# Kernel optimization log

Hardware: AMD Instinct MI355X
Metric: run time of the kernel (lower is better)

Reference implementation:

```python
import jax, jax.numpy as jnp
import numpy as np
from jax import lax

GN_GROUPS = 32
EPS = 1e-5


def conv_gn_silu(x, W, b, scale, bias, stride, padding):
    # Conv2d (OIHW weights, NCHW data) -> GroupNorm(32) -> SiLU
    y = lax.conv_general_dilated(
        x, W, (stride, stride), [(padding, padding), (padding, padding)],
        dimension_numbers=("NCHW", "OIHW", "NCHW")) + b[None, :, None, None]
    B, C, H, Wd = y.shape
    yr = y.reshape(B, GN_GROUPS, C // GN_GROUPS, H, Wd)
    mu = yr.mean(axis=(2, 3, 4), keepdims=True)
    var = yr.var(axis=(2, 3, 4), keepdims=True)
    yn = ((yr - mu) * lax.rsqrt(var + EPS)).reshape(B, C, H, Wd)
    yn = yn * scale[None, :, None, None] + bias[None, :, None, None]
    return yn * jax.nn.sigmoid(yn)  # SiLU


def setup_inputs() -> dict:
    key = jax.random.key(0)
    ks = jax.random.split(key, 8)
    C = 256
    B, H, W = 8, 64, 64
    f = lambda k, shp, s: jax.random.normal(k, shp, dtype=jnp.float32) * s
    return {
        "x": f(ks[0], (B, C, H, W), 1.0),
        "y": f(ks[1], (B, C, H, W), 1.0),
        "Wq": f(ks[2], (C, C, 3, 3), 0.02),
        "bq": jnp.zeros((C,), jnp.float32),
        "gq_scale": jnp.ones((C,), jnp.float32),
        "gq_bias": jnp.zeros((C,), jnp.float32),
        "Wk": f(ks[3], (C, C, 2, 2), 0.02),
        "bk": jnp.zeros((C,), jnp.float32),
        "gk_scale": jnp.ones((C,), jnp.float32),
        "gk_bias": jnp.zeros((C,), jnp.float32),
        "Wv": f(ks[4], (C, C, 2, 2), 0.02),
        "bv": jnp.zeros((C,), jnp.float32),
        "gv_scale": jnp.ones((C,), jnp.float32),
        "gv_bias": jnp.zeros((C,), jnp.float32),
        "gamma": f(ks[5], (1,), 1.0),
    }


def reference(x, y, Wq, bq, gq_scale, gq_bias, Wk, bk, gk_scale, gk_bias,
              Wv, bv, gv_scale, gv_bias, gamma):
    B, C, H, W = x.shape
    sr = 2
    Cq = C  # in_dim // factor, factor=1
    q = conv_gn_silu(x, Wq, bq, gq_scale, gq_bias, stride=1, padding=1)   # [B,Cq,H,W]
    k = conv_gn_silu(y, Wk, bk, gk_scale, gk_bias, stride=sr, padding=0)  # [B,Cq,H/sr,W/sr]
    v = conv_gn_silu(y, Wv, bv, gv_scale, gv_bias, stride=sr, padding=0)  # [B,C,H/sr,W/sr]
    N = H * W
    M = (H // sr) * (W // sr)
    q = q.reshape(B, Cq, N)   # proj_query (pre-permute)
    k = k.reshape(B, Cq, M)   # proj_key
    v = v.reshape(B, C, M)    # proj_value
    scale = 1.0 / np.sqrt(Cq).astype(np.float32)
    energy = jnp.einsum("bcn,bcm->bnm", q, k) * scale       # [B,N,M]
    attn = jax.nn.softmax(energy, axis=-1)                   # softmax over keys
    out = jnp.einsum("bcm,bnm->bcn", v, attn).reshape(B, C, H, W)
    return gamma * out
```

## Files before the change

kernel.cpp:

```cpp
#include <hip/hip_runtime.h>
#include <hip/hip_bf16.h>
#include <math.h>

#define B_ 8
#define C_ 256
#define H_ 64
#define W_ 64
#define N_ 4096
#define M_ 1024
#define HW_ 4096

typedef __attribute__((ext_vector_type(8))) short short8;
typedef __attribute__((ext_vector_type(4))) float f32x4;

__device__ __forceinline__ unsigned short f2bf(float x) {
    unsigned u = __float_as_uint(x);
    u += 0x7fffu + ((u >> 16) & 1u);
    return (unsigned short)(u >> 16);
}
__device__ __forceinline__ float bf2f(unsigned short h) {
    return __uint_as_float(((unsigned)h) << 16);
}

__device__ __forceinline__ void gl_lds16(const unsigned short* g, unsigned short* l) {
    __builtin_amdgcn_global_load_lds(
        (const __attribute__((address_space(1))) unsigned int*)g,
        (__attribute__((address_space(3))) unsigned int*)l, 16, 0, 0);
}

__global__ __launch_bounds__(256) void split_w_tap(
    const float* __restrict__ Wq, unsigned short* __restrict__ wtH,
    unsigned short* __restrict__ wtL)
{
    int co = blockIdx.x, ci = threadIdx.x;
    const float* wp = Wq + ((size_t)co * 256 + ci) * 9;
    #pragma unroll
    for (int tap = 0; tap < 9; ++tap) {
        float v = wp[tap];
        unsigned short h = f2bf(v), l = f2bf(v - bf2f(h));
        size_t o = ((size_t)tap << 16) + ((size_t)co << 8) + ci;
        wtH[o] = h; wtL[o] = l;
    }
}

__global__ __launch_bounds__(256) void split_w2(
    const float* __restrict__ Wsrc, unsigned short* __restrict__ wH,
    unsigned short* __restrict__ wL)
{
    int co = blockIdx.x, ci = threadIdx.x;
    const float* wp = Wsrc + ((size_t)co * 256 + ci) * 4;
    #pragma unroll
    for (int tap = 0; tap < 4; ++tap) {
        float v = wp[tap];
        unsigned short h = f2bf(v), l = f2bf(v - bf2f(h));
        size_t o = ((size_t)tap << 16) + ((size_t)co << 8) + ci;
        wH[o] = h; wL[o] = l;
    }
}

__global__ __launch_bounds__(256) void split_x_pad(
    const float* __restrict__ x, unsigned short* __restrict__ xpH,
    unsigned short* __restrict__ xpL)
{
    __shared__ float tile[64][65];
    int blk = blockIdx.x;
    int b = blk >> 6, h = blk & 63;
    int t = threadIdx.x;
    const float* xb = x + ((size_t)b << 20) + (size_t)h * 64;
    size_t obase = (((size_t)b * 4356) + (size_t)(h + 1) * 66 + 1) * 256;
    unsigned short* oH = xpH + obase;
    unsigned short* oL = xpL + obase;
    for (int cc = 0; cc < 256; cc += 64) {
        int wi = t & 63, cq = t >> 6;
        #pragma unroll
        for (int r = 0; r < 16; ++r) {
            int cl = cq * 16 + r;
            tile[cl][wi] = xb[((size_t)(cc + cl)) * 4096 + wi];
        }
        __syncthreads();
        int cl = t & 63, wq = t >> 6;
        #pragma unroll
        for (int r = 0; r < 16; ++r) {
            int wwi = wq * 16 + r;
            float v = tile[cl][wwi];
            unsigned short hh = f2bf(v), lo = f2bf(v - bf2f(hh));
            size_t o = (size_t)wwi * 256 + cc + cl;
            oH[o] = hh; oL[o] = lo;
        }
        __syncthreads();
    }
}

__global__ __launch_bounds__(256) void split_y_t(
    const float* __restrict__ y, unsigned short* __restrict__ yTh,
    unsigned short* __restrict__ yTl, int b0)
{
    __shared__ float tile[64][65];
    int blk = blockIdx.x;
    int bl = blk >> 6, h = blk & 63;
    int t = threadIdx.x;
    const float* yb = y + ((size_t)(b0 + bl) << 20) + (size_t)h * 64;
    size_t obase = (((size_t)bl << 12) + (size_t)h * 64) * 256;
    unsigned short* oH = yTh + obase;
    unsigned short* oL = yTl + obase;
    for (int cc = 0; cc < 256; cc += 64) {
        int wi = t & 63, cq = t >> 6;
        #pragma unroll
        for (int r = 0; r < 16; ++r) {
            int cl = cq * 16 + r;
            tile[cl][wi] = yb[((size_t)(cc + cl)) * 4096 + wi];
        }
        __syncthreads();
        int cl = t & 63, wq = t >> 6;
        #pragma unroll
        for (int r = 0; r < 16; ++r) {
            int wwi = wq * 16 + r;
            float v = tile[cl][wwi];
            unsigned short hh = f2bf(v), lo = f2bf(v - bf2f(hh));
            size_t o = (size_t)wwi * 256 + cc + cl;
            oH[o] = hh; oL[o] = lo;
        }
        __syncthreads();
    }
}

__global__ __launch_bounds__(256, 2) void conv3x3_mfma(
    const unsigned short* __restrict__ xpH, const unsigned short* __restrict__ xpL,
    const unsigned short* __restrict__ wtH, const unsigned short* __restrict__ wtL,
    const float* __restrict__ bq,
    unsigned short* __restrict__ qH, unsigned short* __restrict__ qL)
{
    __shared__ __align__(16) unsigned short bldsH[272 * 32];
    __shared__ __align__(16) unsigned short bldsL[272 * 32];
    __shared__ __align__(16) unsigned short aldsH[2][128 * 32];
    __shared__ __align__(16) unsigned short aldsL[2][128 * 32];

    int blk = blockIdx.x;
    int bat = blk & 7;
    int rest = blk >> 3;
    int cot = rest & 1;
    int pxt = rest >> 1;
    int t = threadIdx.x;
    int w = t >> 6;
    int wco = w >> 1, wpx = w & 1;
    int lane = t & 63;
    int ll = lane & 15, qd = lane >> 4;
    const int h0 = pxt * 2;
    const int co0b = cot * 128;

    const unsigned short* xpHb = xpH + (size_t)bat * 4356 * 256;
    const unsigned short* xpLb = xpL + (size_t)bat * 4356 * 256;

    f32x4 acc[4][4];
    #pragma unroll
    for (int i = 0; i < 4; ++i)
        #pragma unroll
        for (int j = 0; j < 4; ++j) acc[i][j] = (f32x4){0.f, 0.f, 0.f, 0.f};

    int buf = 0;
    for (int chunk = 0; chunk < 8; ++chunk) {
        const int ci0 = chunk * 32;
        for (int j = w; j < 34; j += 4) {
            int half = (j >= 17);
            int jj = half ? j - 17 : j;
            int gid = jj * 64 + lane;
            int cell = gid >> 2;
            int g = gid & 3;
            int cellc = cell < 264 ? cell : 263;
            int dr = cellc / 66;
            int cc = cellc - dr * 66;
            const unsigned short* src = (half ? xpLb : xpHb)
                + (((size_t)(h0 + dr) * 66 + cc) << 8) + ci0
                + ((g ^ (cellc & 3)) << 3);
            unsigned short* dst = (half ? bldsL : bldsH) + jj * 512;
            gl_lds16(src, dst);
        }
        for (int j = w; j < 16; j += 4) {
            int half = j >> 3;
            int jj = j & 7;
            int gid = jj * 64 + lane;
            int co = gid >> 2;
            int g = gid & 3;
            const unsigned short* src = (half ? wtL : wtH)
                + (((size_t)(co0b + co)) << 8) + ci0 + ((g ^ (co & 3)) << 3);
            unsigned short* dst = (half ? aldsL[buf] : aldsH[buf]) + jj * 512;
            gl_lds16(src, dst);
        }
        __syncthreads();

        for (int tap = 0; tap < 9; ++tap) {
            if (tap < 8) {
                const int aoff = (tap + 1) << 16;
                for (int j = w; j < 16; j += 4) {
                    int half = j >> 3;
                    int jj = j & 7;
                    int gid = jj * 64 + lane;
                    int co = gid >> 2;
                    int g = gid & 3;
                    const unsigned short* src = (half ? wtL : wtH)
                        + aoff + (((size_t)(co0b + co)) << 8) + ci0
                        + ((g ^ (co & 3)) << 3);
                    unsigned short* dst = (half ? aldsL[buf ^ 1] : aldsH[buf ^ 1]) + jj * 512;
                    gl_lds16(src, dst);
                }
            }
            int kh = tap / 3, kw = tap - kh * 3;
            short8 avh[4], avl[4], bvh[4], bvl[4];
            #pragma unroll
            for (int ib = 0; ib < 4; ++ib) {
                int col = wco * 64 + ib * 16 + ll;
                int aa = col * 32 + ((qd ^ (col & 3)) << 3);
                avh[ib] = *(const short8*)&aldsH[buf][aa];
                avl[ib] = *(const short8*)&aldsL[buf][aa];
            }
            #pragma unroll
            for (int jb = 0; jb < 4; ++jb) {
                int cell = (wpx + kh) * 66 + jb * 16 + ll + kw;
                int ba = cell * 32 + ((qd ^ (cell & 3)) << 3);
                bvh[jb] = *(const short8*)&bldsH[ba];
                bvl[jb] = *(const short8*)&bldsL[ba];
            }
            __builtin_amdgcn_s_setprio(1);
            #pragma unroll
            for (int ib = 0; ib < 4; ++ib)
                #pragma unroll
                for (int jb = 0; jb < 4; ++jb) {
                    f32x4 o = acc[ib][jb];
                    o = __builtin_amdgcn_mfma_f32_16x16x32_bf16(avh[ib], bvh[jb], o, 0, 0, 0);
                    o = __builtin_amdgcn_mfma_f32_16x16x32_bf16(avl[ib], bvh[jb], o, 0, 0, 0);
                    o = __builtin_amdgcn_mfma_f32_16x16x32_bf16(avh[ib], bvl[jb], o, 0, 0, 0);
                    acc[ib][jb] = o;
                }
            __builtin_amdgcn_s_setprio(0);
            __syncthreads();
            buf ^= 1;
        }
    }

    const int co0 = cot * 128 + wco * 64;
    const int pxbase = pxt * 128 + wpx * 64;
    #pragma unroll
    for (int ib = 0; ib < 4; ++ib) {
        #pragma unroll
        for (int r = 0; r < 4; ++r) {
            int co = co0 + ib * 16 + qd * 4 + r;
            float bvv = bq[co];
            size_t rowo = ((size_t)(bat * 256 + co)) << 12;
            #pragma unroll
            for (int jb = 0; jb < 4; ++jb) {
                float v = acc[ib][jb][r] + bvv;
                unsigned short h = f2bf(v), l = f2bf(v - bf2f(h));
                size_t o = rowo + pxbase + jb * 16 + ll;
                qH[o] = h; qL[o] = l;
            }
        }
    }
}

__global__ __launch_bounds__(256, 2) void conv2x2_mfma(
    const unsigned short* __restrict__ yTh, const unsigned short* __restrict__ yTl,
    const unsigned short* __restrict__ wkH, const unsigned short* __restrict__ wkL,
    const unsigned short* __restrict__ wvH, const unsigned short* __restrict__ wvL,
    const float* __restrict__ bk, const float* __restrict__ bv,
    float* __restrict__ kf, float* __restrict__ vf, int b0)
{
    __shared__ __align__(16) unsigned short bldsH[512 * 32];
    __shared__ __align__(16) unsigned short bldsL[512 * 32];

    int blk = blockIdx.x;
    int batl = blk & 3;
    int sel = (blk >> 2) & 3;
    int mt  = blk >> 4;
    int t = threadIdx.x;
    int w = t >> 6;
    int wco = w >> 1, wpx = w & 1;
    int lane = t & 63;
    int ll = lane & 15, qd = lane >> 4;

    const unsigned short* wtH_; const unsigned short* wtL_;
    const float* bias; float* dst; int co0;
    if (sel < 2) { wtH_ = wkH; wtL_ = wkL; bias = bk; dst = kf; co0 = sel * 128 + wco * 64; }
    else         { wtH_ = wvH; wtL_ = wvL; bias = bv; dst = vf; co0 = (sel - 2) * 128 + wco * 64; }

    const unsigned short* aHp[4]; const unsigned short* aLp[4];
    #pragma unroll
    for (int ib = 0; ib < 4; ++ib) {
        size_t o = ((size_t)(co0 + ib * 16 + ll)) * 256 + qd * 8;
        aHp[ib] = wtH_ + o; aLp[ib] = wtL_ + o;
    }
    const unsigned short* ySH = yTh + ((((size_t)batl << 12) + mt * 512) << 8);
    const unsigned short* ySL = yTl + ((((size_t)batl << 12) + mt * 512) << 8);
    const int half_ = w >> 1;
    const int gi0 = (w & 1) * 16;
    const unsigned short* yS = half_ ? ySL : ySH;
    unsigned short* bd = half_ ? bldsL : bldsH;
    const int scell = lane >> 2;
    const int sg = lane & 3;

    f32x4 acc[4][4];
    #pragma unroll
    for (int i = 0; i < 4; ++i)
        #pragma unroll
        for (int j = 0; j < 4; ++j) acc[i][j] = (f32x4){0.f, 0.f, 0.f, 0.f};

    for (int chunk = 0; chunk < 8; ++chunk) {
        const int ci0 = chunk * 32;
        #pragma unroll
        for (int j = 0; j < 16; ++j) {
            int gi = gi0 + j;
            int cell = gi * 16 + scell;
            const unsigned short* src = yS + ((size_t)cell << 8) + ci0
                                        + ((sg ^ ((cell >> 1) & 3)) << 3);
            gl_lds16(src, bd + gi * 512);
        }
        __syncthreads();

        #pragma unroll
        for (int tap = 0; tap < 4; ++tap) {
            int kh = tap >> 1, kw = tap & 1;
            const int aoff = (tap << 16) + ci0;
            short8 avh[4], avl[4], bvh[4], bvl[4];
            #pragma unroll
            for (int ib = 0; ib < 4; ++ib) {
                avh[ib] = *(const short8*)(aHp[ib] + aoff);
                avl[ib] = *(const short8*)(aLp[ib] + aoff);
            }
            #pragma unroll
            for (int jb = 0; jb < 4; ++jb) {
                int mlocal = wpx * 64 + jb * 16 + ll;
                int cell = (2 * (mlocal >> 5) + kh) * 64 + 2 * (mlocal & 31) + kw;
                int ba = cell * 32 + ((qd ^ ((cell >> 1) & 3)) << 3);
                bvh[jb] = *(const short8*)&bldsH[ba];
                bvl[jb] = *(const short8*)&bldsL[ba];
            }
            __builtin_amdgcn_s_setprio(1);
            #pragma unroll
            for (int ib = 0; ib < 4; ++ib)
                #pragma unroll
                for (int jb = 0; jb < 4; ++jb) {
                    f32x4 o = acc[ib][jb];
                    o = __builtin_amdgcn_mfma_f32_16x16x32_bf16(avh[ib], bvh[jb], o, 0, 0, 0);
                    o = __builtin_amdgcn_mfma_f32_16x16x32_bf16(avl[ib], bvh[jb], o, 0, 0, 0);
                    o = __builtin_amdgcn_mfma_f32_16x16x32_bf16(avh[ib], bvl[jb], o, 0, 0, 0);
                    acc[ib][jb] = o;
                }
            __builtin_amdgcn_s_setprio(0);
        }
        __syncthreads();
    }

    const int mbase = mt * 128 + wpx * 64;
    #pragma unroll
    for (int ib = 0; ib < 4; ++ib) {
        #pragma unroll
        for (int r = 0; r < 4; ++r) {
            int co = co0 + ib * 16 + qd * 4 + r;
            float bvv = bias[co];
            float* op = dst + (((size_t)((b0 + batl) * 256 + co)) << 10) + mbase + ll;
            #pragma unroll
            for (int jb = 0; jb < 4; ++jb)
                op[jb * 16] = acc[ib][jb][r] + bvv;
        }
    }
}

__global__ __launch_bounds__(256) void gn_stats_kernel(
    const float* __restrict__ buf, float* __restrict__ stats, int S)
{
    int bg = blockIdx.x;
    const float4* p = (const float4*)(buf + (size_t)bg * 8 * S);
    int n4 = 2 * S;
    float s = 0.f, s2 = 0.f;
    for (int i = threadIdx.x; i < n4; i += 256) {
        float4 vv = p[i];
        s  += vv.x + vv.y + vv.z + vv.w;
        s2 += vv.x * vv.x + vv.y * vv.y + vv.z * vv.z + vv.w * vv.w;
    }
    for (int d = 1; d < 64; d <<= 1) { s += __shfl_xor(s, d); s2 += __shfl_xor(s2, d); }
    __shared__ float red[8];
    int w = threadIdx.x >> 6;
    if ((threadIdx.x & 63) == 0) { red[w] = s; red[w + 4] = s2; }
    __syncthreads();
    if (threadIdx.x == 0) {
        s  = red[0] + red[1] + red[2] + red[3];
        s2 = red[4] + red[5] + red[6] + red[7];
        float invn = 1.f / (float)(8 * S);
        float mean = s * invn;
        float var = s2 * invn - mean * mean;
        if (var < 0.f) var = 0.f;
        stats[bg * 2]     = mean;
        stats[bg * 2 + 1] = 1.f / sqrtf(var + 1e-5f);
    }
}

__global__ __launch_bounds__(256) void gn_stats_pair(
    const unsigned short* __restrict__ hi, const unsigned short* __restrict__ lo,
    const float* __restrict__ scale, const float* __restrict__ bias,
    float2* __restrict__ ab, int S)
{
    int bg = blockIdx.x;
    const uint4* ph = (const uint4*)(hi + (size_t)bg * 8 * S);
    const uint4* pl = (const uint4*)(lo + (size_t)bg * 8 * S);
    int n8 = S;
    float s = 0.f, s2 = 0.f;
    for (int i = threadIdx.x; i < n8; i += 256) {
        uint4 a = ph[i], b2 = pl[i];
        unsigned ua[4] = {a.x, a.y, a.z, a.w}, ub[4] = {b2.x, b2.y, b2.z, b2.w};
        #pragma unroll
        for (int j = 0; j < 4; ++j) {
            float x0 = __uint_as_float(ua[j] << 16) + __uint_as_float(ub[j] << 16);
            float x1 = __uint_as_float(ua[j] & 0xffff0000u) + __uint_as_float(ub[j] & 0xffff0000u);
            s += x0 + x1;
            s2 += x0 * x0 + x1 * x1;
        }
    }
    for (int d = 1; d < 64; d <<= 1) { s += __shfl_xor(s, d); s2 += __shfl_xor(s2, d); }
    __shared__ float red[8];
    __shared__ float mv[2];
    int w = threadIdx.x >> 6;
    if ((threadIdx.x & 63) == 0) { red[w] = s; red[w + 4] = s2; }
    __syncthreads();
    if (threadIdx.x == 0) {
        s  = red[0] + red[1] + red[2] + red[3];
        s2 = red[4] + red[5] + red[6] + red[7];
        float invn = 1.f / (float)(8 * S);
        float mean = s * invn;
        float var = s2 * invn - mean * mean;
        if (var < 0.f) var = 0.f;
        mv[0] = mean;
        mv[1] = 1.f / sqrtf(var + 1e-5f);
    }
    __syncthreads();
    if (threadIdx.x < 8) {
        int c = (bg & 31) * 8 + threadIdx.x;
        float a = scale[c] * mv[1];
        float bb = bias[c] - mv[0] * a;
        ab[(bg >> 5) * 256 + c] = make_float2(a, bb);
    }
}

__global__ __launch_bounds__(256) void gn_silu_split_v(
    const float* __restrict__ vf, unsigned short* __restrict__ hi,
    unsigned short* __restrict__ lo, const float* __restrict__ stats,
    const float* __restrict__ scale, const float* __restrict__ bias, int total8)
{
    int idx = blockIdx.x * 256 + threadIdx.x;
    if (idx >= total8) return;
    size_t e = (size_t)idx * 8;
    int c  = (int)((e >> 10) & 255);
    int gg = (int)(e >> 13);
    float mean = stats[gg * 2], rstd = stats[gg * 2 + 1];
    float a  = scale[c] * rstd;
    float bb = bias[c] - mean * a;
    float4 f0 = ((const float4*)vf)[idx * 2];
    float4 f1 = ((const float4*)vf)[idx * 2 + 1];
    float xs[8] = {f0.x, f0.y, f0.z, f0.w, f1.x, f1.y, f1.z, f1.w};
    unsigned oh[4], ol[4];
    #pragma unroll
    for (int j = 0; j < 4; ++j) {
        float y0 = xs[2 * j] * a + bb, y1 = xs[2 * j + 1] * a + bb;
        float s0 = y0 / (1.f + __expf(-y0));
        float s1 = y1 / (1.f + __expf(-y1));
        unsigned short h0 = f2bf(s0), l0 = f2bf(s0 - bf2f(h0));
        unsigned short h1 = f2bf(s1), l1 = f2bf(s1 - bf2f(h1));
        oh[j] = h0 | ((unsigned)h1 << 16);
        ol[j] = l0 | ((unsigned)l1 << 16);
    }
    ((uint4*)hi)[idx] = make_uint4(oh[0], oh[1], oh[2], oh[3]);
    ((uint4*)lo)[idx] = make_uint4(ol[0], ol[1], ol[2], ol[3]);
}

__global__ __launch_bounds__(256) void gn_silu_split_kT(
    const float* __restrict__ kf, unsigned short* __restrict__ th,
    unsigned short* __restrict__ tl, const float* __restrict__ stats,
    const float* __restrict__ scale, const float* __restrict__ bias)
{
    int bm = blockIdx.x;
    int b = bm >> 7, m8 = (bm & 127) * 8;
    int c = threadIdx.x;
    int gg = b * 32 + (c >> 3);
    float mean = stats[gg * 2], rstd = stats[gg * 2 + 1];
    float a  = scale[c] * rstd;
    float bb = bias[c] - mean * a;
    const float* src = kf + (((size_t)(b * 256 + c)) << 10) + m8;
    float4 f0 = *(const float4*)src;
    float4 f1 = *(const float4*)(src + 4);
    float xs[8] = {f0.x, f0.y, f0.z, f0.w, f1.x, f1.y, f1.z, f1.w};
    #pragma unroll
    for (int j = 0; j < 8; ++j) {
        float y = xs[j] * a + bb;
        float s = y / (1.f + __expf(-y));
        unsigned short h = f2bf(s), l = f2bf(s - bf2f(h));
        size_t o = ((size_t)b * M_ + m8 + j) * C_ + c;
        th[o] = h;
        tl[o] = l;
    }
}

__global__ __launch_bounds__(256, 2) void attn_mfma(
    const unsigned short* __restrict__ qh, const unsigned short* __restrict__ qlo,
    const unsigned short* __restrict__ kth, const unsigned short* __restrict__ ktl,
    const unsigned short* __restrict__ vh, const unsigned short* __restrict__ vlo,
    const float2* __restrict__ abq,
    const float* __restrict__ gamma, float* __restrict__ out)
{
    __shared__ __align__(16) unsigned short kldsH[32 * 256];
    __shared__ __align__(16) unsigned short kldsL[32 * 256];
    __shared__ __align__(16) unsigned short vldsH[256 * 32];
    __shared__ __align__(16) unsigned short vldsL[256 * 32];
    __shared__ __align__(16) unsigned short pH[4][16][40];
    __shared__ __align__(16) unsigned short pL[4][16][40];
    __shared__ float alphaS[4][16];

    int blk = blockIdx.x;
    int bat = blk & 7;
    int nt  = blk >> 3;
    int t = threadIdx.x;
    int w = t >> 6;
    int lane = t & 63;
    int ll = lane & 15;
    int qd = lane >> 4;
    int n0 = nt * 64 + w * 16;

    short8 aqh[8], aql[8];
    {
        const unsigned short* qb1 = qh  + (size_t)bat * C_ * N_ + n0 + ll;
        const unsigned short* qb2 = qlo + (size_t)bat * C_ * N_ + n0 + ll;
        const float2* ab = abq + bat * 256;
        #pragma unroll
        for (int ks = 0; ks < 8; ++ks) {
            #pragma unroll
            for (int j = 0; j < 8; ++j) {
                int c = ks * 32 + qd * 8 + j;
                size_t off = (size_t)c * N_;
                float xv = bf2f(qb1[off]) + bf2f(qb2[off]);
                float2 t2 = ab[c];
                float yv = xv * t2.x + t2.y;
                float sv = 0.0625f * yv / (1.f + __expf(-yv));
                unsigned short h = f2bf(sv);
                aqh[ks][j] = (short)h;
                aql[ks][j] = (short)f2bf(sv - bf2f(h));
            }
        }
    }

    f32x4 oacc[16];
    #pragma unroll
    for (int i = 0; i < 16; ++i) oacc[i] = (f32x4){0.f, 0.f, 0.f, 0.f};
    f32x4 lacc = (f32x4){0.f, 0.f, 0.f, 0.f};
    float mrun[4] = {-3e38f, -3e38f, -3e38f, -3e38f};
    const short8 ones = (short8){16256, 16256, 16256, 16256, 16256, 16256, 16256, 16256};

    const unsigned short* kg = ((w & 1) == 0 ? kth : ktl) + (size_t)bat * M_ * C_;
    const unsigned short* vg = ((w & 1) == 0 ? vh  : vlo) + (size_t)bat * C_ * M_;
    unsigned short* kdst = (w & 1) ? kldsL : kldsH;
    unsigned short* vdst = (w & 1) ? vldsL : vldsH;
    const int krow  = lane >> 5;
    const int kcolg = lane & 31;
    const int vc_l  = lane >> 2;
    const int vg_g  = lane & 3;

    for (int mt = 0; mt < 32; ++mt) {
        const int m0 = mt * 32;
        if (w < 2) {
            #pragma unroll
            for (int i = 0; i < 16; ++i) {
                int row = 2 * i + krow;
                const unsigned short* src = kg + (size_t)(m0 + row) * 256
                                            + ((kcolg ^ (row & 7)) << 3);
                gl_lds16(src, kdst + i * 512);
            }
        } else {
            #pragma unroll
            for (int i = 0; i < 16; ++i) {
                int c = i * 16 + vc_l;
                const unsigned short* src = vg + (size_t)c * M_ + m0
                                            + ((vg_g ^ ((c >> 1) & 3)) << 3);
                gl_lds16(src, vdst + i * 512);
            }
        }
        __syncthreads();

        f32x4 s0 = {0.f, 0.f, 0.f, 0.f}, s1 = {0.f, 0.f, 0.f, 0.f};
        __builtin_amdgcn_s_setprio(1);
        #pragma unroll
        for (int ks = 0; ks < 8; ++ks) {
            int cg = ks * 4 + qd;
            int a0 = ll * 256 + ((cg ^ (ll & 7)) << 3);
            int a1 = (ll + 16) * 256 + ((cg ^ (ll & 7)) << 3);
            short8 b0h = *(const short8*)&kldsH[a0];
            short8 b1h = *(const short8*)&kldsH[a1];
            short8 b0l = *(const short8*)&kldsL[a0];
            short8 b1l = *(const short8*)&kldsL[a1];
            s0 = __builtin_amdgcn_mfma_f32_16x16x32_bf16(aqh[ks], b0h, s0, 0, 0, 0);
            s1 = __builtin_amdgcn_mfma_f32_16x16x32_bf16(aqh[ks], b1h, s1, 0, 0, 0);
            s0 = __builtin_amdgcn_mfma_f32_16x16x32_bf16(aql[ks], b0h, s0, 0, 0, 0);
            s1 = __builtin_amdgcn_mfma_f32_16x16x32_bf16(aql[ks], b1h, s1, 0, 0, 0);
            s0 = __builtin_amdgcn_mfma_f32_16x16x32_bf16(aqh[ks], b0l, s0, 0, 0, 0);
            s1 = __builtin_amdgcn_mfma_f32_16x16x32_bf16(aqh[ks], b1l, s1, 0, 0, 0);
        }
        __builtin_amdgcn_s_setprio(0);

        float alpha4[4];
        #pragma unroll
        for (int r = 0; r < 4; ++r) {
            float mx = fmaxf(s0[r], s1[r]);
            mx = fmaxf(mx, __shfl_xor(mx, 1));
            mx = fmaxf(mx, __shfl_xor(mx, 2));
            mx = fmaxf(mx, __shfl_xor(mx, 4));
            mx = fmaxf(mx, __shfl_xor(mx, 8));
            float mn = fmaxf(mrun[r], mx);
            float al = __expf(mrun[r] - mn);
            mrun[r] = mn;
            float p0 = __expf(s0[r] - mn);
            float p1 = __expf(s1[r] - mn);
            alpha4[r] = al;
            unsigned short h0 = f2bf(p0), l0 = f2bf(p0 - bf2f(h0));
            unsigned short h1 = f2bf(p1), l1 = f2bf(p1 - bf2f(h1));
            int rn = qd * 4 + r;
            pH[w][rn][ll] = h0;  pH[w][rn][16 + ll] = h1;
            pL[w][rn][ll] = l0;  pL[w][rn][16 + ll] = l1;
        }
        if (ll == 0) {
            #pragma unroll
            for (int r = 0; r < 4; ++r) alphaS[w][qd * 4 + r] = alpha4[r];
        }
        __builtin_amdgcn_wave_barrier();
        short8 bph = *(const short8*)&pH[w][ll][qd * 8];
        short8 bpl = *(const short8*)&pL[w][ll][qd * 8];
        float an = alphaS[w][ll];
        {
            f32x4 o = lacc;
            o[0] *= an; o[1] *= an; o[2] *= an; o[3] *= an;
            o = __builtin_amdgcn_mfma_f32_16x16x32_bf16(ones, bph, o, 0, 0, 0);
            o = __builtin_amdgcn_mfma_f32_16x16x32_bf16(ones, bpl, o, 0, 0, 0);
            lacc = o;
        }
        __builtin_amdgcn_s_setprio(1);
        #pragma unroll
        for (int ct = 0; ct < 16; ++ct) {
            int c = ct * 16 + ll;
            int av = c * 32 + ((qd ^ ((c >> 1) & 3)) << 3);
            short8 avh = *(const short8*)&vldsH[av];
            short8 avl = *(const short8*)&vldsL[av];
            f32x4 o = oacc[ct];
            o[0] *= an; o[1] *= an; o[2] *= an; o[3] *= an;
            o = __builtin_amdgcn_mfma_f32_16x16x32_bf16(avh, bph, o, 0, 0, 0);
            o = __builtin_amdgcn_mfma_f32_16x16x32_bf16(avl, bph, o, 0, 0, 0);
            o = __builtin_amdgcn_mfma_f32_16x16x32_bf16(avh, bpl, o, 0, 0, 0);
            oacc[ct] = o;
        }
        __builtin_amdgcn_s_setprio(0);
        __syncthreads();
    }

    float linv = gamma[0] / lacc[0];
    float* ob = out + (size_t)bat * C_ * N_ + n0 + ll;
    #pragma unroll
    for (int ct = 0; ct < 16; ++ct) {
        #pragma unroll
        for (int r = 0; r < 4; ++r) {
            int c = ct * 16 + qd * 4 + r;
            ob[(size_t)c * N_] = oacc[ct][r] * linv;
        }
    }
}

extern "C" void kernel_launch(void* const* d_in, const int* in_sizes, int n_in,
                              void* d_out, int out_size, void* d_ws, size_t ws_size,
                              hipStream_t stream)
{
    const float* x   = (const float*)d_in[0];
    const float* y   = (const float*)d_in[1];
    const float* Wq  = (const float*)d_in[2];
    const float* bq  = (const float*)d_in[3];
    const float* gqs = (const float*)d_in[4];
    const float* gqb = (const float*)d_in[5];
    const float* Wk  = (const float*)d_in[6];
    const float* bk  = (const float*)d_in[7];
    const float* gks = (const float*)d_in[8];
    const float* gkb = (const float*)d_in[9];
    const float* Wv  = (const float*)d_in[10];
    const float* bv  = (const float*)d_in[11];
    const float* gvs = (const float*)d_in[12];
    const float* gvb = (const float*)d_in[13];
    const float* gamma = (const float*)d_in[14];
    float* out = (float*)d_out;

    char* base = (char*)d_ws;
    unsigned short* qH = (unsigned short*)base;
    unsigned short* qL = qH + 8388608;
    char* regA = (char*)(qL + 8388608);
    unsigned short* xpH = (unsigned short*)regA;
    unsigned short* xpL = xpH + 8921088;
    unsigned short* wtH = xpL + 8921088;
    unsigned short* wtL = wtH + 589824;
    float* kf = (float*)regA;
    float* vf = kf + 2097152;
    unsigned short* kTh = (unsigned short*)(vf + 2097152);
    unsigned short* kTl = kTh + 2097152;
    unsigned short* vH  = kTl + 2097152;
    unsigned short* vL  = vH + 2097152;
    float* stq = (float*)(vL + 2097152);
    float* stk = stq + 512;
    float* stv = stk + 512;
    float2* abq = (float2*)(stv + 512);
    unsigned short* yTh  = (unsigned short*)(vf + 2097152);
    unsigned short* yTl  = yTh + 4194304;
    unsigned short* w2kH = yTl + 4194304;
    unsigned short* w2kL = w2kH + 262144;
    unsigned short* w2vH = w2kL + 262144;
    unsigned short* w2vL = w2vH + 262144;

    hipMemsetAsync(xpH, 0, (size_t)2 * 8921088 * sizeof(unsigned short), stream);
    split_w_tap<<<256, 256, 0, stream>>>(Wq, wtH, wtL);
    split_x_pad<<<512, 256, 0, stream>>>(x, xpH, xpL);
    conv3x3_mfma<<<512, 256, 0, stream>>>(xpH, xpL, wtH, wtL, bq, qH, qL);

    split_w2<<<256, 256, 0, stream>>>(Wk, w2kH, w2kL);
    split_w2<<<256, 256, 0, stream>>>(Wv, w2vH, w2vL);
    split_y_t<<<256, 256, 0, stream>>>(y, yTh, yTl, 0);
    conv2x2_mfma<<<128, 256, 0, stream>>>(yTh, yTl, w2kH, w2kL, w2vH, w2vL,
                                          bk, bv, kf, vf, 0);
    split_y_t<<<256, 256, 0, stream>>>(y, yTh, yTl, 4);
    conv2x2_mfma<<<128, 256, 0, stream>>>(yTh, yTl, w2kH, w2kL, w2vH, w2vL,
                                          bk, bv, kf, vf, 4);

    gn_stats_pair<<<256, 256, 0, stream>>>(qH, qL, gqs, gqb, abq, 4096);
    gn_stats_kernel<<<256, 256, 0, stream>>>(kf, stk, 1024);
    gn_stats_kernel<<<256, 256, 0, stream>>>(vf, stv, 1024);
    gn_silu_split_v<<<1024, 256, 0, stream>>>(vf, vH, vL, stv, gvs, gvb, 262144);
    gn_silu_split_kT<<<1024, 256, 0, stream>>>(kf, kTh, kTl, stk, gks, gkb);
    attn_mfma<<<512, 256, 0, stream>>>(qH, qL, kTh, kTl, vH, vL, abq, gamma, out);
}
```

Baseline: 505.8 us.

## Double-buffer K/V tiles, use 512-thread blocks, and skip most softmax rescales

The attention kernel now runs 8 waves per block over 128 query rows, so each staged K/V tile is shared by more waves. K/V tiles are double-buffered in LDS, with the next tile prefetched while the current one is computed, and the per-tile sync moves to the end of the loop. The three split-precision score MFMAs accumulate into separate registers to shorten dependency chains. Online-softmax rescaling is skipped unless a wave's row max grows by more than 8, which cuts multiplies but lets unnormalized exponentials reach up to e^8. LDS use doubles, which may limit occupancy.

```diff
diff --git a/kernel.cpp b/kernel.cpp
--- a/kernel.cpp
+++ b/kernel.cpp
@@ -11,6 +11,7 @@
 #define HW_ 4096
 
 typedef __attribute__((ext_vector_type(8))) short short8;
+typedef __attribute__((ext_vector_type(4))) short short4v;
 typedef __attribute__((ext_vector_type(4))) float f32x4;
 
 __device__ __forceinline__ unsigned short f2bf(float x) {
@@ -497,20 +498,20 @@
     }
 }
 
-__global__ __launch_bounds__(256, 2) void attn_mfma(
+__global__ __launch_bounds__(512, 2) void attn_mfma(
     const unsigned short* __restrict__ qh, const unsigned short* __restrict__ qlo,
     const unsigned short* __restrict__ kth, const unsigned short* __restrict__ ktl,
     const unsigned short* __restrict__ vh, const unsigned short* __restrict__ vlo,
     const float2* __restrict__ abq,
     const float* __restrict__ gamma, float* __restrict__ out)
 {
-    __shared__ __align__(16) unsigned short kldsH[32 * 256];
-    __shared__ __align__(16) unsigned short kldsL[32 * 256];
-    __shared__ __align__(16) unsigned short vldsH[256 * 32];
-    __shared__ __align__(16) unsigned short vldsL[256 * 32];
-    __shared__ __align__(16) unsigned short pH[4][16][40];
-    __shared__ __align__(16) unsigned short pL[4][16][40];
-    __shared__ float alphaS[4][16];
+    __shared__ __align__(16) unsigned short kldsH[2][32 * 256];
+    __shared__ __align__(16) unsigned short kldsL[2][32 * 256];
+    __shared__ __align__(16) unsigned short vldsH[2][256 * 32];
+    __shared__ __align__(16) unsigned short vldsL[2][256 * 32];
+    __shared__ __align__(16) unsigned short pH[8][16][36];
+    __shared__ __align__(16) unsigned short pL[8][16][36];
+    __shared__ float alphaS[8][16];
 
     int blk = blockIdx.x;
     int bat = blk & 7;
@@ -520,7 +521,41 @@
     int lane = t & 63;
     int ll = lane & 15;
     int qd = lane >> 4;
-    int n0 = nt * 64 + w * 16;
+    int n0 = nt * 128 + w * 16;
+
+    const unsigned short* kg = ((w & 1) == 0 ? kth : ktl) + (size_t)bat * M_ * C_;
+    const unsigned short* vg = ((w & 1) == 0 ? vh  : vlo) + (size_t)bat * C_ * M_;
+    const int krow  = lane >> 5;
+    const int kcolg = lane & 31;
+    const int vc_l  = lane >> 2;
+    const int vg_g  = lane & 3;
+    const int ihalf = (w >> 2) * 8;
+
+    auto stage = [&](int m0, int b) {
+        if ((w & 2) == 0) {
+            unsigned short* kd = (w & 1) ? kldsL[b] : kldsH[b];
+            #pragma unroll
+            for (int j = 0; j < 8; ++j) {
+                int i = ihalf + j;
+                int row = 2 * i + krow;
+                const unsigned short* src = kg + (size_t)(m0 + row) * 256
+                                            + ((kcolg ^ (row & 7)) << 3);
+                gl_lds16(src, kd + i * 512);
+            }
+        } else {
+            unsigned short* vd = (w & 1) ? vldsL[b] : vldsH[b];
+            #pragma unroll
+            for (int j = 0; j < 8; ++j) {
+                int i = ihalf + j;
+                int c = i * 16 + vc_l;
+                const unsigned short* src = vg + (size_t)c * M_ + m0
+                                            + ((vg_g ^ ((c >> 1) & 3)) << 3);
+                gl_lds16(src, vd + i * 512);
+            }
+        }
+    };
+
+    stage(0, 0);
 
     short8 aqh[8], aql[8];
     {
@@ -551,57 +586,37 @@
     float mrun[4] = {-3e38f, -3e38f, -3e38f, -3e38f};
     const short8 ones = (short8){16256, 16256, 16256, 16256, 16256, 16256, 16256, 16256};
 
-    const unsigned short* kg = ((w & 1) == 0 ? kth : ktl) + (size_t)bat * M_ * C_;
-    const unsigned short* vg = ((w & 1) == 0 ? vh  : vlo) + (size_t)bat * C_ * M_;
-    unsigned short* kdst = (w & 1) ? kldsL : kldsH;
-    unsigned short* vdst = (w & 1) ? vldsL : vldsH;
-    const int krow  = lane >> 5;
-    const int kcolg = lane & 31;
-    const int vc_l  = lane >> 2;
-    const int vg_g  = lane & 3;
+    __syncthreads();
 
     for (int mt = 0; mt < 32; ++mt) {
-        const int m0 = mt * 32;
-        if (w < 2) {
-            #pragma unroll
-            for (int i = 0; i < 16; ++i) {
-                int row = 2 * i + krow;
-                const unsigned short* src = kg + (size_t)(m0 + row) * 256
-                                            + ((kcolg ^ (row & 7)) << 3);
-                gl_lds16(src, kdst + i * 512);
-            }
-        } else {
-            #pragma unroll
-            for (int i = 0; i < 16; ++i) {
-                int c = i * 16 + vc_l;
-                const unsigned short* src = vg + (size_t)c * M_ + m0
-                                            + ((vg_g ^ ((c >> 1) & 3)) << 3);
-                gl_lds16(src, vdst + i * 512);
-            }
-        }
-        __syncthreads();
+        const int cur = mt & 1;
+        if (mt < 31) stage((mt + 1) * 32, cur ^ 1);
 
         f32x4 s0 = {0.f, 0.f, 0.f, 0.f}, s1 = {0.f, 0.f, 0.f, 0.f};
+        f32x4 s0b = {0.f, 0.f, 0.f, 0.f}, s1b = {0.f, 0.f, 0.f, 0.f};
+        f32x4 s0c = {0.f, 0.f, 0.f, 0.f}, s1c = {0.f, 0.f, 0.f, 0.f};
         __builtin_amdgcn_s_setprio(1);
         #pragma unroll
         for (int ks = 0; ks < 8; ++ks) {
             int cg = ks * 4 + qd;
             int a0 = ll * 256 + ((cg ^ (ll & 7)) << 3);
             int a1 = (ll + 16) * 256 + ((cg ^ (ll & 7)) << 3);
-            short8 b0h = *(const short8*)&kldsH[a0];
-            short8 b1h = *(const short8*)&kldsH[a1];
-            short8 b0l = *(const short8*)&kldsL[a0];
-            short8 b1l = *(const short8*)&kldsL[a1];
-            s0 = __builtin_amdgcn_mfma_f32_16x16x32_bf16(aqh[ks], b0h, s0, 0, 0, 0);
-            s1 = __builtin_amdgcn_mfma_f32_16x16x32_bf16(aqh[ks], b1h, s1, 0, 0, 0);
-            s0 = __builtin_amdgcn_mfma_f32_16x16x32_bf16(aql[ks], b0h, s0, 0, 0, 0);
-            s1 = __builtin_amdgcn_mfma_f32_16x16x32_bf16(aql[ks], b1h, s1, 0, 0, 0);
-            s0 = __builtin_amdgcn_mfma_f32_16x16x32_bf16(aqh[ks], b0l, s0, 0, 0, 0);
-            s1 = __builtin_amdgcn_mfma_f32_16x16x32_bf16(aqh[ks], b1l, s1, 0, 0, 0);
+            short8 b0h = *(const short8*)&kldsH[cur][a0];
+            short8 b1h = *(const short8*)&kldsH[cur][a1];
+            short8 b0l = *(const short8*)&kldsL[cur][a0];
+            short8 b1l = *(const short8*)&kldsL[cur][a1];
+            s0  = __builtin_amdgcn_mfma_f32_16x16x32_bf16(aqh[ks], b0h, s0, 0, 0, 0);
+            s1  = __builtin_amdgcn_mfma_f32_16x16x32_bf16(aqh[ks], b1h, s1, 0, 0, 0);
+            s0b = __builtin_amdgcn_mfma_f32_16x16x32_bf16(aql[ks], b0h, s0b, 0, 0, 0);
+            s1b = __builtin_amdgcn_mfma_f32_16x16x32_bf16(aql[ks], b1h, s1b, 0, 0, 0);
+            s0c = __builtin_amdgcn_mfma_f32_16x16x32_bf16(aqh[ks], b0l, s0c, 0, 0, 0);
+            s1c = __builtin_amdgcn_mfma_f32_16x16x32_bf16(aqh[ks], b1l, s1c, 0, 0, 0);
         }
         __builtin_amdgcn_s_setprio(0);
-
-        float alpha4[4];
+        s0 = s0 + s0b + s0c;
+        s1 = s1 + s1b + s1c;
+
+        float mx4[4];
         #pragma unroll
         for (int r = 0; r < 4; ++r) {
             float mx = fmaxf(s0[r], s1[r]);
@@ -609,46 +624,81 @@
             mx = fmaxf(mx, __shfl_xor(mx, 2));
             mx = fmaxf(mx, __shfl_xor(mx, 4));
             mx = fmaxf(mx, __shfl_xor(mx, 8));
-            float mn = fmaxf(mrun[r], mx);
-            float al = __expf(mrun[r] - mn);
-            mrun[r] = mn;
-            float p0 = __expf(s0[r] - mn);
-            float p1 = __expf(s1[r] - mn);
-            alpha4[r] = al;
+            mx4[r] = mx;
+        }
+        bool grow = (mx4[0] > mrun[0] + 8.f) | (mx4[1] > mrun[1] + 8.f) |
+                    (mx4[2] > mrun[2] + 8.f) | (mx4[3] > mrun[3] + 8.f);
+        const bool resc = __any(grow);
+        if (resc) {
+            float alpha4[4];
+            #pragma unroll
+            for (int r = 0; r < 4; ++r) {
+                float mn = fmaxf(mrun[r], mx4[r]);
+                alpha4[r] = __expf(mrun[r] - mn);
+                mrun[r] = mn;
+            }
+            if (ll == 0) {
+                #pragma unroll
+                for (int r = 0; r < 4; ++r) alphaS[w][qd * 4 + r] = alpha4[r];
+            }
+        }
+        #pragma unroll
+        for (int r = 0; r < 4; ++r) {
+            float p0 = __expf(s0[r] - mrun[r]);
+            float p1 = __expf(s1[r] - mrun[r]);
             unsigned short h0 = f2bf(p0), l0 = f2bf(p0 - bf2f(h0));
             unsigned short h1 = f2bf(p1), l1 = f2bf(p1 - bf2f(h1));
             int rn = qd * 4 + r;
             pH[w][rn][ll] = h0;  pH[w][rn][16 + ll] = h1;
             pL[w][rn][ll] = l0;  pL[w][rn][16 + ll] = l1;
         }
-        if (ll == 0) {
-            #pragma unroll
-            for (int r = 0; r < 4; ++r) alphaS[w][qd * 4 + r] = alpha4[r];
-        }
         __builtin_amdgcn_wave_barrier();
-        short8 bph = *(const short8*)&pH[w][ll][qd * 8];
-        short8 bpl = *(const short8*)&pL[w][ll][qd * 8];
-        float an = alphaS[w][ll];
-        {
-            f32x4 o = lacc;
-            o[0] *= an; o[1] *= an; o[2] *= an; o[3] *= an;
-            o = __builtin_amdgcn_mfma_f32_16x16x32_bf16(ones, bph, o, 0, 0, 0);
-            o = __builtin_amdgcn_mfma_f32_16x16x32_bf16(ones, bpl, o, 0, 0, 0);
-            lacc = o;
-        }
+
+        short4v ph0 = *(const short4v*)&pH[w][ll][qd * 8];
+        short4v ph1 = *(const short4v*)&pH[w][ll][qd * 8 + 4];
+        short4v pl0 = *(const short4v*)&pL[w][ll][qd * 8];
+        short4v pl1 = *(const short4v*)&pL[w][ll][qd * 8 + 4];
+        short8 bph = __builtin_shufflevector(ph0, ph1, 0, 1, 2, 3, 4, 5, 6, 7);
+        short8 bpl = __builtin_shufflevector(pl0, pl1, 0, 1, 2, 3, 4, 5, 6, 7);
+
         __builtin_amdgcn_s_setprio(1);
-        #pragma unroll
-        for (int ct = 0; ct < 16; ++ct) {
-            int c = ct * 16 + ll;
-            int av = c * 32 + ((qd ^ ((c >> 1) & 3)) << 3);
-            short8 avh = *(const short8*)&vldsH[av];
-            short8 avl = *(const short8*)&vldsL[av];
-            f32x4 o = oacc[ct];
-            o[0] *= an; o[1] *= an; o[2] *= an; o[3] *= an;
-            o = __builtin_amdgcn_mfma_f32_16x16x32_bf16(avh, bph, o, 0, 0, 0);
-            o = __builtin_amdgcn_mfma_f32_16x16x32_bf16(avl, bph, o, 0, 0, 0);
-            o = __builtin_amdgcn_mfma_f32_16x16x32_bf16(avh, bpl, o, 0, 0, 0);
-            oacc[ct] = o;
+        if (resc) {
+            float an = alphaS[w][ll];
+            {
+                f32x4 o = lacc;
+                o[0] *= an; o[1] *= an; o[2] *= an; o[3] *= an;
+                o = __builtin_amdgcn_mfma_f32_16x16x32_bf16(ones, bph, o, 0, 0, 0);
+                o = __builtin_amdgcn_mfma_f32_16x16x32_bf16(ones, bpl, o, 0, 0, 0);
+                lacc = o;
+            }
+            #pragma unroll
+            for (int ct = 0; ct < 16; ++ct) {
+                int c = ct * 16 + ll;
+                int av = c * 32 + ((qd ^ ((c >> 1) & 3)) << 3);
+                short8 avh = *(const short8*)&vldsH[cur][av];
+                short8 avl = *(const short8*)&vldsL[cur][av];
+                f32x4 o = oacc[ct];
+                o[0] *= an; o[1] *= an; o[2] *= an; o[3] *= an;
+                o = __builtin_amdgcn_mfma_f32_16x16x32_bf16(avh, bph, o, 0, 0, 0);
+                o = __builtin_amdgcn_mfma_f32_16x16x32_bf16(avl, bph, o, 0, 0, 0);
+                o = __builtin_amdgcn_mfma_f32_16x16x32_bf16(avh, bpl, o, 0, 0, 0);
+                oacc[ct] = o;
+            }
+        } else {
+            lacc = __builtin_amdgcn_mfma_f32_16x16x32_bf16(ones, bph, lacc, 0, 0, 0);
+            lacc = __builtin_amdgcn_mfma_f32_16x16x32_bf16(ones, bpl, lacc, 0, 0, 0);
+            #pragma unroll
+            for (int ct = 0; ct < 16; ++ct) {
+                int c = ct * 16 + ll;
+                int av = c * 32 + ((qd ^ ((c >> 1) & 3)) << 3);
+                short8 avh = *(const short8*)&vldsH[cur][av];
+                short8 avl = *(const short8*)&vldsL[cur][av];
+                f32x4 o = oacc[ct];
+                o = __builtin_amdgcn_mfma_f32_16x16x32_bf16(avh, bph, o, 0, 0, 0);
+                o = __builtin_amdgcn_mfma_f32_16x16x32_bf16(avl, bph, o, 0, 0, 0);
+                o = __builtin_amdgcn_mfma_f32_16x16x32_bf16(avh, bpl, o, 0, 0, 0);
+                oacc[ct] = o;
+            }
         }
         __builtin_amdgcn_s_setprio(0);
         __syncthreads();
@@ -731,5 +781,5 @@
     gn_stats_kernel<<<256, 256, 0, stream>>>(vf, stv, 1024);
     gn_silu_split_v<<<1024, 256, 0, stream>>>(vf, vH, vL, stv, gvs, gvb, 262144);
     gn_silu_split_kT<<<1024, 256, 0, stream>>>(kf, kTh, kTl, stk, gks, gkb);
-    attn_mfma<<<512, 256, 0, stream>>>(qH, qL, kTh, kTl, vH, vL, abq, gamma, out);
-}
+    attn_mfma<<<256, 512, 0, stream>>>(qH, qL, kTh, kTl, vH, vL, abq, gamma, out);
+}
```

Result: slower. 596.6 us (+18.0%).
